# Optimization experiments

Measured on AMD Instinct MI355X. Metric: run time of the kernel, lower is better.

The kernel has to match this reference:

```python
import jax, jax.numpy as jnp
import numpy as np

N = 50000   # nodes
E = 160000  # edges
B = 32      # graphs in batch
C1 = N // 2   # clusters after first graclus pool
C2 = C1 // 2  # clusters after second graclus pool
IN, H1, H2, HID, FC, OUT = 32, 32, 64, 25, 128, 32


def _seg_max(x, idx, n):
    r = jax.ops.segment_max(x, idx, num_segments=n)
    return jnp.where(jnp.isfinite(r), r, 0.0)  # empty segments -> 0 (torch_scatter fill)


def _nnconv(x, src, dst, ea, w1, b1, w2, b2, root, bias, in_c, out_c, n, self_mask=None):
    # per-edge weight matrix from edge MLP: [E, in_c, out_c]
    We = (jax.nn.relu(ea @ w1 + b1) @ w2 + b2).reshape(-1, in_c, out_c)
    msg = jnp.einsum('ei,eio->eo', x[src], We)  # gather + batched matvec
    if self_mask is not None:  # emulate remove_self_loops after pooling
        msg = jnp.where(self_mask[:, None], -jnp.inf, msg)
    return _seg_max(msg, dst, n) + x @ root + bias  # scatter-max + root weight


def _cartesian(pos, src, dst):
    # T.Cartesian(cat=False, norm=True): relative pos scaled to [0,1]
    cart = pos[dst] - pos[src]
    return cart / (2.0 * jnp.max(jnp.abs(cart))) + 0.5


def setup_inputs() -> dict:
    key = jax.random.key(0)
    ks = jax.random.split(key, 16)
    x = jax.random.normal(ks[0], (N, IN), jnp.float32)
    pos = jax.random.uniform(ks[1], (N, 2), jnp.float32)
    edge_attr = jax.random.uniform(ks[2], (E, 2), jnp.float32)
    edge_index = jax.random.randint(ks[3], (2, E), 0, N)
    batch = jnp.sort(jax.random.randint(ks[4], (N,), 0, B))
    # graclus stand-in clusters (pairwise matching -> non-empty, batch-consistent)
    cluster1 = jnp.arange(N, dtype=jnp.int32) // 2
    cluster2 = jnp.arange(C1, dtype=jnp.int32) // 2

    def lin(k, i, o):
        return jax.random.normal(k, (i, o), jnp.float32) / np.sqrt(i).astype(np.float32)

    params = dict(
        nn1_w1=lin(ks[5], 2, HID), nn1_b1=jnp.zeros((HID,), jnp.float32),
        nn1_w2=lin(ks[6], HID, IN * H1), nn1_b2=jnp.zeros((IN * H1,), jnp.float32),
        root1=lin(ks[7], IN, H1), bias1=jnp.zeros((H1,), jnp.float32),
        nn2_w1=lin(ks[8], 2, HID), nn2_b1=jnp.zeros((HID,), jnp.float32),
        nn2_w2=lin(ks[9], HID, H1 * H2), nn2_b2=jnp.zeros((H1 * H2,), jnp.float32),
        root2=lin(ks[10], H1, H2), bias2=jnp.zeros((H2,), jnp.float32),
        fc1_w=lin(ks[11], H2, FC), fc1_b=jnp.zeros((FC,), jnp.float32),
        fc2_w=lin(ks[12], FC, OUT), fc2_b=jnp.zeros((OUT,), jnp.float32),
    )
    return dict(x=x, pos=pos, edge_attr=edge_attr, edge_index=edge_index,
                batch=batch, cluster1=cluster1, cluster2=cluster2, **params)


def reference(x, pos, edge_attr, edge_index, batch, cluster1, cluster2,
              nn1_w1, nn1_b1, nn1_w2, nn1_b2, root1, bias1,
              nn2_w1, nn2_b1, nn2_w2, nn2_b2, root2, bias2,
              fc1_w, fc1_b, fc2_w, fc2_b):
    src, dst = edge_index[0], edge_index[1]
    # conv1 (NNConv, aggr='max') + elu
    x1 = jax.nn.elu(_nnconv(x, src, dst, edge_attr,
                            nn1_w1, nn1_b1, nn1_w2, nn1_b2, root1, bias1, IN, H1, N))
    # max_pool(cluster1): x by max, pos by mean, batch carried, edges relabeled
    x2 = _seg_max(x1, cluster1, C1)
    cnt = jax.ops.segment_sum(jnp.ones((N,), x.dtype), cluster1, num_segments=C1)
    pos2 = jax.ops.segment_sum(pos, cluster1, num_segments=C1) / jnp.maximum(cnt, 1.0)[:, None]
    batch2 = jax.ops.segment_max(batch, cluster1, num_segments=C1)
    src2, dst2 = cluster1[src], cluster1[dst]
    ea2 = _cartesian(pos2, src2, dst2)  # transform=T.Cartesian on pooled graph
    # conv2 + elu (self-loops created by pooling are masked out of the max-aggr)
    x3 = jax.nn.elu(_nnconv(x2, src2, dst2, ea2,
                            nn2_w1, nn2_b1, nn2_w2, nn2_b2, root2, bias2, H1, H2, C1,
                            self_mask=(src2 == dst2)))
    # max_pool_x(cluster2)
    x4 = _seg_max(x3, cluster2, C2)
    batch3 = jax.ops.segment_max(batch2, cluster2, num_segments=C2)
    # global_mean_pool
    s = jax.ops.segment_sum(x4, batch3, num_segments=B)
    c = jax.ops.segment_sum(jnp.ones((C2,), x.dtype), batch3, num_segments=B)
    g = s / jnp.maximum(c, 1.0)[:, None]
    h = jax.nn.elu(g @ fc1_w + fc1_b)  # dropout is identity in eval mode
    return jax.nn.log_softmax(h @ fc2_w + fc2_b, axis=1)
```

## Files before the change

kernel.cpp:

```cpp
#include <hip/hip_runtime.h>
#include <math.h>

#define N_NODES 50000
#define N_EDGES 160000
#define NB 32
#define C1N 25000
#define C2N 12500
#define EPB 128
#define GPB 128

#define OFF_AGG1 0
#define SZ_AGG1 (N_NODES*32)
#define OFF_AGG2 (OFF_AGG1+SZ_AGG1)
#define SZ_AGG2  (C1N*64)
#define NEG_TOTAL (OFF_AGG2+SZ_AGG2)
#define OFF_GSUM NEG_TOTAL
#define OFF_GCNT (OFF_GSUM + NB*64)
#define OFF_CMAX (OFF_GCNT + NB)
#define ZERO_END (OFF_CMAX + 4)
#define OFF_X2   ZERO_END
#define OFF_POS2 (OFF_X2 + C1N*32)
#define OFF_X4   (OFF_POS2 + C1N*2)
#define OFF_CART (OFF_X4 + C2N*64)
#define OFF_BB1  (OFF_CART + N_EDGES*2)
#define OFF_BB2  (OFF_BB1 + 13312)

typedef __attribute__((ext_vector_type(8))) short short8;
typedef __attribute__((ext_vector_type(4))) float f32x4;

__device__ __forceinline__ void atomicMaxFloat(float* addr, float v) {
    if (v >= 0.0f) atomicMax((int*)addr, __float_as_int(v + 0.0f));
    else           atomicMin((unsigned int*)addr, __float_as_uint(v));
}
__device__ __forceinline__ float eluf(float v) { return v > 0.0f ? v : expm1f(v); }
__device__ __forceinline__ unsigned short f2bf(float f) {
    unsigned int u = __float_as_uint(f);
    u += 0x7FFFu + ((u >> 16) & 1u);
    return (unsigned short)(u >> 16);
}

__global__ void k_init(float* ws) {
    int i = blockIdx.x*256 + threadIdx.x;
    if (i < ZERO_END) ws[i] = (i < NEG_TOTAL) ? -__builtin_inff() : 0.0f;
}

template<int O>
__global__ void k_swzf(const float* __restrict__ w2, const float* __restrict__ b2,
                       unsigned short* __restrict__ Bf) {
    const int TOT = 26*(O/16)*512;
    int idx = blockIdx.x*256 + threadIdx.x;
    if (idx >= TOT) return;
    int t = idx >> 9;
    int l = (idx >> 3) & 63, j = idx & 7;
    int h = t / (O/16), ntg = t % (O/16);
    int i = (l >> 4)*8 + j;
    int o = ntg*16 + (l & 15);
    float v = (h < 25) ? w2[h*(32*O) + i*O + o] : b2[i*O + o];
    Bf[idx] = f2bf(v);
}

template<int O, int NTILES, int NTOFF_T, int SELF, int HASCM, int SHIFT>
__global__ __launch_bounds__(512, 4) void k_edgemm(
    const float* __restrict__ X, const unsigned short* __restrict__ Bf,
    const float* __restrict__ w1, const float* __restrict__ b1,
    const int* __restrict__ srcArr, const int* __restrict__ dstArr,
    const float* __restrict__ eaArr, const float* __restrict__ cmaxp,
    float* __restrict__ agg)
{
    __shared__ __align__(16) unsigned short Wl[26*NTILES*512];
    __shared__ int src_s[EPB], dst_s[EPB];
    int tid = threadIdx.x;
    int e0 = blockIdx.x * EPB;
    if (tid < EPB) {
        int s = srcArr[e0+tid], d = dstArr[e0+tid];
        if (SHIFT) { s >>= 1; d >>= 1; }
        src_s[tid] = s; dst_s[tid] = d;
    }
    const int NU4 = 26*NTILES*64;
    for (int idx = tid; idx < NU4; idx += 512) {
        int q = idx & 63, nt = (idx >> 6) % NTILES, h = idx / (64*NTILES);
        ((uint4*)Wl)[idx] = ((const uint4*)Bf)[(h*(O/16) + NTOFF_T + nt)*64 + q];
    }
    float sc = 1.0f, off = 0.0f;
    if (HASCM) { sc = 0.5f / *cmaxp; off = 0.5f; }
    int l = tid & 63, w = tid >> 6;
    int erow = w*16 + (l & 15);
    int i0 = (l >> 4) * 8;
    int e = e0 + erow;
    float a0 = eaArr[e*2]   * sc + off;
    float a1 = eaArr[e*2+1] * sc + off;
    __syncthreads();
    const float* xr = X + (size_t)src_s[erow]*32 + i0;
    float xv[8];
    *(float4*)&xv[0] = *(const float4*)xr;
    *(float4*)&xv[4] = *(const float4*)(xr + 4);
    f32x4 acc[NTILES];
    #pragma unroll
    for (int nt = 0; nt < NTILES; ++nt) acc[nt] = (f32x4){0.f,0.f,0.f,0.f};
    for (int h = 0; h < 26; ++h) {
        float rv = (h < 25) ? fmaxf(a0*w1[h] + a1*w1[25+h] + b1[h], 0.0f) : 1.0f;
        union { short8 s8; unsigned int u[4]; } av;
        #pragma unroll
        for (int p = 0; p < 4; ++p) {
            float lo = xv[2*p]   * rv;
            float hi = xv[2*p+1] * rv;
            asm("v_cvt_pk_bf16_f32 %0, %1, %2" : "=v"(av.u[p]) : "v"(lo), "v"(hi));
        }
        #pragma unroll
        for (int nt = 0; nt < NTILES; ++nt) {
            short8 bv = *(const short8*)&Wl[(h*NTILES + nt)*512 + l*8];
            acc[nt] = __builtin_amdgcn_mfma_f32_16x16x32_bf16(av.s8, bv, acc[nt], 0, 0, 0);
        }
    }
    int colb = NTOFF_T*16 + (l & 15);
    #pragma unroll
    for (int nt = 0; nt < NTILES; ++nt) {
        #pragma unroll
        for (int r = 0; r < 4; ++r) {
            int er = w*16 + (l >> 4)*4 + r;
            int d = dst_s[er];
            if (!SELF || src_s[er] != d)
                atomicMaxFloat(&agg[(size_t)d*O + colb + nt*16], acc[nt][r]);
        }
    }
}

__global__ __launch_bounds__(256) void k_x2(const float* __restrict__ x,
                                            const float* __restrict__ pos,
                                            const float* __restrict__ root1,
                                            const float* __restrict__ bias1,
                                            float* ws) {
    __shared__ float xs[512];
    int tid = threadIdx.x;
    int n0 = blockIdx.x*16;
    for (int idx = tid; idx < 512; idx += 256) xs[idx] = x[n0*32 + idx];
    __syncthreads();
    int o = tid & 31, ci = tid >> 5;
    int c = blockIdx.x*8 + ci;
    float b = bias1[o];
    float acc0 = b, acc1 = b;
    const float* x0 = xs + (2*ci)*32;
    const float* x1 = xs + (2*ci+1)*32;
    #pragma unroll
    for (int i = 0; i < 32; ++i) {
        float rw = root1[i*32+o];
        acc0 += x0[i]*rw; acc1 += x1[i]*rw;
    }
    float v0 = ws[OFF_AGG1 + (size_t)(2*c)*32 + o];
    float v1 = ws[OFF_AGG1 + (size_t)(2*c+1)*32 + o];
    if (v0 == -__builtin_inff()) v0 = 0.0f;
    if (v1 == -__builtin_inff()) v1 = 0.0f;
    v0 = eluf(v0 + acc0); v1 = eluf(v1 + acc1);
    ws[OFF_X2 + c*32 + o] = fmaxf(v0, v1);
    if (o < 2) ws[OFF_POS2 + c*2 + o] = 0.5f*(pos[(2*c)*2 + o] + pos[(2*c+1)*2 + o]);
}

__global__ void k_cart(const int* __restrict__ eidx, float* ws) {
    int e = blockIdx.x*256 + threadIdx.x;
    float m = 0.0f;
    if (e < N_EDGES) {
        int s2 = eidx[e] >> 1, d2 = eidx[N_EDGES+e] >> 1;
        float cx = ws[OFF_POS2 + d2*2]     - ws[OFF_POS2 + s2*2];
        float cy = ws[OFF_POS2 + d2*2 + 1] - ws[OFF_POS2 + s2*2 + 1];
        ws[OFF_CART + e*2] = cx; ws[OFF_CART + e*2 + 1] = cy;
        m = fmaxf(fabsf(cx), fabsf(cy));
    }
    #pragma unroll
    for (int off = 32; off; off >>= 1) m = fmaxf(m, __shfl_xor(m, off));
    if ((threadIdx.x & 63) == 0) atomicMax((int*)(ws+OFF_CMAX), __float_as_int(m));
}

__global__ __launch_bounds__(256) void k_x4(const float* __restrict__ root2,
                                            const float* __restrict__ bias2,
                                            float* ws) {
    __shared__ float xs[256];
    int tid = threadIdx.x;
    int r0 = blockIdx.x*8;
    xs[tid] = ws[OFF_X2 + r0*32 + tid];
    __syncthreads();
    int o = tid & 63, ci = tid >> 6;
    int c2 = blockIdx.x*4 + ci;
    float b = bias2[o];
    float acc0 = b, acc1 = b;
    const float* x0 = xs + (2*ci)*32;
    const float* x1 = xs + (2*ci+1)*32;
    #pragma unroll
    for (int i = 0; i < 32; ++i) {
        float rw = root2[i*64+o];
        acc0 += x0[i]*rw; acc1 += x1[i]*rw;
    }
    float v0 = ws[OFF_AGG2 + (size_t)(2*c2)*64 + o];
    float v1 = ws[OFF_AGG2 + (size_t)(2*c2+1)*64 + o];
    if (v0 == -__builtin_inff()) v0 = 0.0f;
    if (v1 == -__builtin_inff()) v1 = 0.0f;
    v0 = eluf(v0 + acc0); v1 = eluf(v1 + acc1);
    ws[OFF_X4 + c2*64 + o] = fmaxf(v0, v1);
}

__global__ __launch_bounds__(256) void k_gpool(const int* __restrict__ batch, float* ws) {
    int tid = threadIdx.x;
    int o = tid & 63, cl = tid >> 6;
    const int CPB = (C2N + GPB - 1) / GPB;
    int c0 = blockIdx.x * CPB;
    int c1 = c0 + CPB; if (c1 > C2N) c1 = C2N;
    float acc = 0.0f, cnt = 0.0f;
    int curb = -1;
    for (int c = c0 + cl; c < c1; c += 4) {
        int b = batch[4*c + 3];
        float v = ws[OFF_X4 + c*64 + o];
        if (b != curb) {
            if (curb >= 0) {
                atomicAdd(&ws[OFF_GSUM + curb*64 + o], acc);
                if (o == 0) atomicAdd(&ws[OFF_GCNT + curb], cnt);
            }
            curb = b; acc = 0.0f; cnt = 0.0f;
        }
        acc += v; cnt += 1.0f;
    }
    if (curb >= 0) {
        atomicAdd(&ws[OFF_GSUM + curb*64 + o], acc);
        if (o == 0) atomicAdd(&ws[OFF_GCNT + curb], cnt);
    }
}

__global__ __launch_bounds__(256) void k_head(
    const float* __restrict__ fc1w, const float* __restrict__ fc1b,
    const float* __restrict__ fc2w, const float* __restrict__ fc2b,
    const float* __restrict__ ws, float* __restrict__ out) {
    __shared__ float g_s[32*64], h_s[32*128], l_s[32*32];
    int tid = threadIdx.x;
    for (int idx = tid; idx < 32*64; idx += 256) {
        int b = idx >> 6;
        g_s[idx] = ws[OFF_GSUM + idx] / fmaxf(ws[OFF_GCNT + b], 1.0f);
    }
    __syncthreads();
    for (int idx = tid; idx < 32*128; idx += 256) {
        int b = idx >> 7, f = idx & 127;
        float a = fc1b[f];
        #pragma unroll 8
        for (int i = 0; i < 64; ++i) a += g_s[b*64+i]*fc1w[i*128+f];
        h_s[idx] = eluf(a);
    }
    __syncthreads();
    for (int idx = tid; idx < 32*32; idx += 256) {
        int b = idx >> 5, o = idx & 31;
        float a = fc2b[o];
        #pragma unroll 8
        for (int i = 0; i < 128; ++i) a += h_s[b*128+i]*fc2w[i*32+o];
        l_s[idx] = a;
    }
    __syncthreads();
    if (tid < 32) {
        int b = tid;
        float m = -__builtin_inff();
        for (int o = 0; o < 32; ++o) m = fmaxf(m, l_s[b*32+o]);
        float s = 0.0f;
        for (int o = 0; o < 32; ++o) s += expf(l_s[b*32+o]-m);
        float lg = logf(s);
        for (int o = 0; o < 32; ++o) out[b*32+o] = l_s[b*32+o]-m-lg;
    }
}

extern "C" void kernel_launch(void* const* d_in, const int* in_sizes, int n_in,
                              void* d_out, int out_size, void* d_ws, size_t ws_size,
                              hipStream_t stream) {
    const float* x    = (const float*)d_in[0];
    const float* pos  = (const float*)d_in[1];
    const float* ea   = (const float*)d_in[2];
    const int*   eidx = (const int*)  d_in[3];
    const int*   batch= (const int*)  d_in[4];
    const float* n1w1 = (const float*)d_in[7];
    const float* n1b1 = (const float*)d_in[8];
    const float* n1w2 = (const float*)d_in[9];
    const float* n1b2 = (const float*)d_in[10];
    const float* root1= (const float*)d_in[11];
    const float* bias1= (const float*)d_in[12];
    const float* n2w1 = (const float*)d_in[13];
    const float* n2b1 = (const float*)d_in[14];
    const float* n2w2 = (const float*)d_in[15];
    const float* n2b2 = (const float*)d_in[16];
    const float* root2= (const float*)d_in[17];
    const float* bias2= (const float*)d_in[18];
    const float* fc1w = (const float*)d_in[19];
    const float* fc1b = (const float*)d_in[20];
    const float* fc2w = (const float*)d_in[21];
    const float* fc2b = (const float*)d_in[22];
    float* ws  = (float*)d_ws;
    float* out = (float*)d_out;
    unsigned short* Bb1 = (unsigned short*)(ws + OFF_BB1);
    unsigned short* Bb2 = (unsigned short*)(ws + OFF_BB2);

    hipLaunchKernelGGL(k_init, dim3((ZERO_END+255)/256), dim3(256), 0, stream, ws);
    hipLaunchKernelGGL((k_swzf<32>), dim3(104), dim3(256), 0, stream, n1w2, n1b2, Bb1);
    hipLaunchKernelGGL((k_swzf<64>), dim3(208), dim3(256), 0, stream, n2w2, n2b2, Bb2);
    hipLaunchKernelGGL((k_edgemm<32, 2, 0, 0, 0, 0>), dim3(N_EDGES/EPB), dim3(512), 0, stream,
                       x, Bb1, n1w1, n1b1, eidx, eidx + N_EDGES, ea,
                       (const float*)nullptr, ws + OFF_AGG1);
    hipLaunchKernelGGL(k_x2, dim3(C1N/8), dim3(256), 0, stream, x, pos, root1, bias1, ws);
    hipLaunchKernelGGL(k_cart, dim3(N_EDGES/256), dim3(256), 0, stream, eidx, ws);
    hipLaunchKernelGGL((k_edgemm<64, 2, 0, 1, 1, 1>), dim3(N_EDGES/EPB), dim3(512), 0, stream,
                       ws + OFF_X2, Bb2, n2w1, n2b1, eidx, eidx + N_EDGES,
                       ws + OFF_CART, ws + OFF_CMAX, ws + OFF_AGG2);
    hipLaunchKernelGGL((k_edgemm<64, 2, 2, 1, 1, 1>), dim3(N_EDGES/EPB), dim3(512), 0, stream,
                       ws + OFF_X2, Bb2, n2w1, n2b1, eidx, eidx + N_EDGES,
                       ws + OFF_CART, ws + OFF_CMAX, ws + OFF_AGG2);
    hipLaunchKernelGGL(k_x4, dim3(C2N/4), dim3(256), 0, stream, root2, bias2, ws);
    hipLaunchKernelGGL(k_gpool, dim3(GPB), dim3(256), 0, stream, batch, ws);
    hipLaunchKernelGGL(k_head, dim3(1), dim3(256), 0, stream,
                       fc1w, fc1b, fc2w, fc2b, ws, out);
}
```

Measured before the change: 307.8 us.

## Sort edges by destination via counting sort and pre-reduce atomic max runs

Adds a histogram, a single-block prefix scan and a scatter pass that build a destination-sorted permutation of the edges. The edge-MLP kernels then process edges in that order. Each lane combines consecutive rows that share a destination before issuing one atomic max, which cuts atomic traffic and improves locality of the scatter-max. The cost is three extra kernels, including a serial 1024-thread scan, plus indirect gathers of src, dst and edge attributes through the permutation.

```diff
diff --git a/kernel.cpp b/kernel.cpp
--- a/kernel.cpp
+++ b/kernel.cpp
@@ -17,8 +17,10 @@
 #define OFF_GSUM NEG_TOTAL
 #define OFF_GCNT (OFF_GSUM + NB*64)
 #define OFF_CMAX (OFF_GCNT + NB)
-#define ZERO_END (OFF_CMAX + 4)
-#define OFF_X2   ZERO_END
+#define OFF_HIST (OFF_CMAX + 4)
+#define ZERO_END (OFF_HIST + N_NODES)
+#define OFF_PERM ZERO_END
+#define OFF_X2   (OFF_PERM + N_EDGES)
 #define OFF_POS2 (OFF_X2 + C1N*32)
 #define OFF_X4   (OFF_POS2 + C1N*2)
 #define OFF_CART (OFF_X4 + C2N*64)
@@ -42,6 +44,44 @@
 __global__ void k_init(float* ws) {
     int i = blockIdx.x*256 + threadIdx.x;
     if (i < ZERO_END) ws[i] = (i < NEG_TOTAL) ? -__builtin_inff() : 0.0f;
+}
+
+__global__ void k_hist(const int* __restrict__ dstArr, float* ws) {
+    int e = blockIdx.x*256 + threadIdx.x;
+    if (e < N_EDGES) atomicAdd((int*)(ws+OFF_HIST) + dstArr[e], 1);
+}
+
+__global__ __launch_bounds__(1024) void k_scan(float* ws) {
+    int* hist = (int*)(ws + OFF_HIST);
+    __shared__ int part[1024];
+    int t = threadIdx.x;
+    const int PER = (N_NODES + 1023) / 1024;
+    int base = t*PER;
+    int s = 0;
+    for (int i = 0; i < PER; ++i) {
+        int idx = base + i;
+        if (idx < N_NODES) s += hist[idx];
+    }
+    part[t] = s; __syncthreads();
+    for (int off = 1; off < 1024; off <<= 1) {
+        int v = (t >= off) ? part[t-off] : 0;
+        __syncthreads();
+        part[t] += v;
+        __syncthreads();
+    }
+    int running = part[t] - s;
+    for (int i = 0; i < PER; ++i) {
+        int idx = base + i;
+        if (idx < N_NODES) { int h = hist[idx]; hist[idx] = running; running += h; }
+    }
+}
+
+__global__ void k_scatter(const int* __restrict__ dstArr, float* ws) {
+    int e = blockIdx.x*256 + threadIdx.x;
+    if (e < N_EDGES) {
+        int p = atomicAdd((int*)(ws+OFF_HIST) + dstArr[e], 1);
+        ((int*)(ws+OFF_PERM))[p] = e;
+    }
 }
 
 template<int O>
@@ -64,17 +104,19 @@
     const float* __restrict__ X, const unsigned short* __restrict__ Bf,
     const float* __restrict__ w1, const float* __restrict__ b1,
     const int* __restrict__ srcArr, const int* __restrict__ dstArr,
+    const int* __restrict__ permArr,
     const float* __restrict__ eaArr, const float* __restrict__ cmaxp,
     float* __restrict__ agg)
 {
     __shared__ __align__(16) unsigned short Wl[26*NTILES*512];
-    __shared__ int src_s[EPB], dst_s[EPB];
+    __shared__ int src_s[EPB], dst_s[EPB], eid_s[EPB];
     int tid = threadIdx.x;
     int e0 = blockIdx.x * EPB;
     if (tid < EPB) {
-        int s = srcArr[e0+tid], d = dstArr[e0+tid];
+        int e = permArr[e0+tid];
+        int s = srcArr[e], d = dstArr[e];
         if (SHIFT) { s >>= 1; d >>= 1; }
-        src_s[tid] = s; dst_s[tid] = d;
+        src_s[tid] = s; dst_s[tid] = d; eid_s[tid] = e;
     }
     const int NU4 = 26*NTILES*64;
     for (int idx = tid; idx < NU4; idx += 512) {
@@ -86,10 +128,10 @@
     int l = tid & 63, w = tid >> 6;
     int erow = w*16 + (l & 15);
     int i0 = (l >> 4) * 8;
-    int e = e0 + erow;
-    float a0 = eaArr[e*2]   * sc + off;
-    float a1 = eaArr[e*2+1] * sc + off;
-    __syncthreads();
+    __syncthreads();
+    int eO = eid_s[erow];
+    float a0 = eaArr[eO*2]   * sc + off;
+    float a1 = eaArr[eO*2+1] * sc + off;
     const float* xr = X + (size_t)src_s[erow]*32 + i0;
     float xv[8];
     *(float4*)&xv[0] = *(const float4*)xr;
@@ -113,15 +155,21 @@
         }
     }
     int colb = NTOFF_T*16 + (l & 15);
+    int er0 = w*16 + (l >> 4)*4;
     #pragma unroll
     for (int nt = 0; nt < NTILES; ++nt) {
+        float* col = agg + colb + nt*16;
+        float m; int prevd;
         #pragma unroll
         for (int r = 0; r < 4; ++r) {
-            int er = w*16 + (l >> 4)*4 + r;
-            int d = dst_s[er];
-            if (!SELF || src_s[er] != d)
-                atomicMaxFloat(&agg[(size_t)d*O + colb + nt*16], acc[nt][r]);
+            int d = dst_s[er0 + r];
+            float v = acc[nt][r];
+            if (SELF && src_s[er0 + r] == d) v = -__builtin_inff();
+            if (r == 0) { prevd = d; m = v; }
+            else if (d == prevd) m = fmaxf(m, v);
+            else { atomicMaxFloat(col + (size_t)prevd*O, m); prevd = d; m = v; }
         }
+        atomicMaxFloat(col + (size_t)prevd*O, m);
     }
 }
 
@@ -289,20 +337,25 @@
     float* out = (float*)d_out;
     unsigned short* Bb1 = (unsigned short*)(ws + OFF_BB1);
     unsigned short* Bb2 = (unsigned short*)(ws + OFF_BB2);
+    const int* dstArr = eidx + N_EDGES;
+    const int* perm   = (const int*)(ws + OFF_PERM);
 
     hipLaunchKernelGGL(k_init, dim3((ZERO_END+255)/256), dim3(256), 0, stream, ws);
     hipLaunchKernelGGL((k_swzf<32>), dim3(104), dim3(256), 0, stream, n1w2, n1b2, Bb1);
     hipLaunchKernelGGL((k_swzf<64>), dim3(208), dim3(256), 0, stream, n2w2, n2b2, Bb2);
+    hipLaunchKernelGGL(k_hist, dim3((N_EDGES+255)/256), dim3(256), 0, stream, dstArr, ws);
+    hipLaunchKernelGGL(k_scan, dim3(1), dim3(1024), 0, stream, ws);
+    hipLaunchKernelGGL(k_scatter, dim3((N_EDGES+255)/256), dim3(256), 0, stream, dstArr, ws);
     hipLaunchKernelGGL((k_edgemm<32, 2, 0, 0, 0, 0>), dim3(N_EDGES/EPB), dim3(512), 0, stream,
-                       x, Bb1, n1w1, n1b1, eidx, eidx + N_EDGES, ea,
+                       x, Bb1, n1w1, n1b1, eidx, dstArr, perm, ea,
                        (const float*)nullptr, ws + OFF_AGG1);
     hipLaunchKernelGGL(k_x2, dim3(C1N/8), dim3(256), 0, stream, x, pos, root1, bias1, ws);
     hipLaunchKernelGGL(k_cart, dim3(N_EDGES/256), dim3(256), 0, stream, eidx, ws);
     hipLaunchKernelGGL((k_edgemm<64, 2, 0, 1, 1, 1>), dim3(N_EDGES/EPB), dim3(512), 0, stream,
-                       ws + OFF_X2, Bb2, n2w1, n2b1, eidx, eidx + N_EDGES,
+                       ws + OFF_X2, Bb2, n2w1, n2b1, eidx, dstArr, perm,
                        ws + OFF_CART, ws + OFF_CMAX, ws + OFF_AGG2);
     hipLaunchKernelGGL((k_edgemm<64, 2, 2, 1, 1, 1>), dim3(N_EDGES/EPB), dim3(512), 0, stream,
-                       ws + OFF_X2, Bb2, n2w1, n2b1, eidx, eidx + N_EDGES,
+                       ws + OFF_X2, Bb2, n2w1, n2b1, eidx, dstArr, perm,
                        ws + OFF_CART, ws + OFF_CMAX, ws + OFF_AGG2);
     hipLaunchKernelGGL(k_x4, dim3(C2N/4), dim3(256), 0, stream, root2, bias2, ws);
     hipLaunchKernelGGL(k_gpool, dim3(GPB), dim3(256), 0, stream, batch, ws);
```

Measured after the change: 387.9 us. +26.0%, slower.
